# Performance work log

Hardware: AMD Instinct MI355X
Metric: run time of the kernel (lower is better)

The kernel has to match this reference:

```python
import jax, jax.numpy as jnp
import numpy as np

EPS = 1e-5

def setup_inputs() -> dict:
    key = jax.random.key(0)
    ks = jax.random.split(key, 5)
    B, C_clip, Hc, Wc = 8, 768, 24, 24
    C_rs, Hr, Wr = 256, 64, 64
    clip_feat = jax.random.normal(ks[0], (B, C_clip, Hc, Wc), dtype=jnp.float32)
    rs_feat = jax.random.normal(ks[1], (B, C_rs, Hr, Wr), dtype=jnp.float32)
    ln_gamma = jnp.ones((C_clip,), dtype=jnp.float32)
    ln_beta = jnp.zeros((C_clip,), dtype=jnp.float32)
    W = jax.random.normal(ks[2], (C_rs, C_clip), dtype=jnp.float32) * (1.0 / np.sqrt(C_clip))
    b = jax.random.normal(ks[3], (C_rs,), dtype=jnp.float32) * 0.01
    alpha = jnp.array([0.5], dtype=jnp.float32)
    return {"clip_feat": clip_feat, "rs_feat": rs_feat, "ln_gamma": ln_gamma,
            "ln_beta": ln_beta, "W": W, "b": b, "alpha": alpha}

def reference(clip_feat, rs_feat, ln_gamma, ln_beta, W, b, alpha):
    B, C_clip, Hc, Wc = clip_feat.shape
    _, C_rs, Hr, Wr = rs_feat.shape
    # tokens: [B, N_clip, C_clip]
    clip_flat = clip_feat.reshape(B, C_clip, Hc * Wc).transpose(0, 2, 1)
    mu = jnp.mean(clip_flat, axis=-1, keepdims=True)
    var = jnp.var(clip_flat, axis=-1, keepdims=True)
    clip_norm = (clip_flat - mu) * jax.lax.rsqrt(var + EPS) * ln_gamma + ln_beta
    # projection to rs_dim: [B, N_clip, C_rs]
    clip_proj = jnp.einsum('bnc,dc->bnd', clip_norm, W) + b
    # rs tokens: [B, N_rs, C_rs]
    rs_flat = rs_feat.reshape(B, C_rs, Hr * Wr).transpose(0, 2, 1)
    # attn_map: [B, N_clip, N_rs], softmax over N_clip (axis=1)
    attn = jnp.einsum('bnd,bmd->bnm', clip_proj, rs_flat)
    attn = jax.nn.softmax(attn, axis=1)
    # attended: [B, N_rs, C_rs]
    attended = jnp.einsum('bnm,bnd->bmd', attn, clip_proj)
    attended = attended.transpose(0, 2, 1).reshape(B, C_rs, Hr, Wr)
    return rs_feat + alpha * attended
```

## Files before the change

kernel.cpp:

```cpp
#include <hip/hip_runtime.h>
#include <hip/hip_bf16.h>

#define EPSF 1e-5f
#define SM_OFF 60.0f

typedef short short8 __attribute__((ext_vector_type(8)));
typedef float f32x4 __attribute__((ext_vector_type(4)));

__device__ __forceinline__ short f2bf(float x) {
    __hip_bfloat16 h = __float2bfloat16(x);
    return reinterpret_cast<short&>(h);
}
__device__ __forceinline__ float bf2f(short s) {
    __hip_bfloat16 h = reinterpret_cast<__hip_bfloat16&>(s);
    return __bfloat162float(h);
}
__device__ __forceinline__ unsigned int pk2(float lo, float hi) {
    return (unsigned int)(unsigned short)f2bf(lo)
         | ((unsigned int)(unsigned short)f2bf(hi) << 16);
}

__global__ __launch_bounds__(256) void w_pack_kernel(
    const float* __restrict__ W,
    short* __restrict__ Wp_hi,
    short* __restrict__ Wp_lo)
{
    int t = blockIdx.x * 256 + threadIdx.x;
    int l15 = t & 15;
    int g   = (t >> 4) & 3;
    int kt  = (t >> 6) % 24;
    int nt  = t / 1536;
    const float* src = W + (size_t)(16 * nt + l15) * 768 + 32 * kt + 8 * g;
    short8 h8, l8;
    #pragma unroll
    for (int j = 0; j < 8; ++j) {
        float w = src[j];
        short h = f2bf(w);
        h8[j] = h;
        l8[j] = f2bf(w - bf2f(h));
    }
    *reinterpret_cast<short8*>(Wp_hi + (size_t)t * 8) = h8;
    *reinterpret_cast<short8*>(Wp_lo + (size_t)t * 8) = l8;
}

__global__ __launch_bounds__(512) void ln_proj_kernel(
    const float* __restrict__ clip,
    const float* __restrict__ gamma,
    const float* __restrict__ beta,
    const short* __restrict__ Wp_hi,
    const short* __restrict__ Wp_lo,
    const float* __restrict__ bias,
    short* __restrict__ proj,
    short* __restrict__ projT)
{
    __shared__ short xh[16][776];
    __shared__ short xl[16][776];
    __shared__ float redA[8][16];
    __shared__ float redB[8][16];
    __shared__ float muS[16], rsS[16];

    const int tid = threadIdx.x;
    const int b  = blockIdx.x / 36;
    const int n0 = (blockIdx.x % 36) * 16;
    const int nl = tid & 15;
    const int cg = tid >> 4;
    const int w  = tid >> 6;
    const int l  = tid & 63;
    const int l15 = l & 15;
    const int g  = l >> 4;

    const float* base = clip + (size_t)b * 768 * 576 + n0 + nl;

    float x[24];
    float s1 = 0.f, s2 = 0.f;
    #pragma unroll
    for (int i = 0; i < 24; ++i) {
        x[i] = base[(size_t)(cg + 32 * i) * 576];
        s1 += x[i]; s2 += x[i] * x[i];
    }
    s1 += __shfl_xor(s1, 16); s2 += __shfl_xor(s2, 16);
    s1 += __shfl_xor(s1, 32); s2 += __shfl_xor(s2, 32);
    if (g == 0) { redA[w][l15] = s1; redB[w][l15] = s2; }
    __syncthreads();
    if (tid < 16) {
        float a = 0.f, q = 0.f;
        #pragma unroll
        for (int k = 0; k < 8; ++k) { a += redA[k][tid]; q += redB[k][tid]; }
        float mu = a * (1.f / 768.f);
        float var = q * (1.f / 768.f) - mu * mu;
        muS[tid] = mu; rsS[tid] = rsqrtf(var + EPSF);
    }
    __syncthreads();
    {
        float mu = muS[nl], rsg = rsS[nl];
        #pragma unroll
        for (int i = 0; i < 24; ++i) {
            int c = cg + 32 * i;
            float y = (x[i] - mu) * rsg * gamma[c] + beta[c];
            short hh = f2bf(y);
            xh[nl][c] = hh;
            xl[nl][c] = f2bf(y - bf2f(hh));
        }
    }
    __syncthreads();

    f32x4 acc[2];
    acc[0] = f32x4{0.f,0.f,0.f,0.f};
    acc[1] = f32x4{0.f,0.f,0.f,0.f};
    for (int kt = 0; kt < 24; ++kt) {
        short8 ah = *reinterpret_cast<const short8*>(&xh[l15][32 * kt + 8 * g]);
        short8 al = *reinterpret_cast<const short8*>(&xl[l15][32 * kt + 8 * g]);
        #pragma unroll
        for (int j = 0; j < 2; ++j) {
            int nt = 2 * w + j;
            size_t off = ((size_t)((nt * 24 + kt) * 64 + l)) * 8;
            short8 bh = *reinterpret_cast<const short8*>(Wp_hi + off);
            short8 bl = *reinterpret_cast<const short8*>(Wp_lo + off);
            acc[j] = __builtin_amdgcn_mfma_f32_16x16x32_bf16(ah, bh, acc[j], 0, 0, 0);
            acc[j] = __builtin_amdgcn_mfma_f32_16x16x32_bf16(al, bh, acc[j], 0, 0, 0);
            acc[j] = __builtin_amdgcn_mfma_f32_16x16x32_bf16(ah, bl, acc[j], 0, 0, 0);
        }
    }

    #pragma unroll
    for (int j = 0; j < 2; ++j) {
        int d = 16 * (2 * w + j) + l15;
        float bb = bias[d];
        #pragma unroll
        for (int r = 0; r < 4; ++r) {
            int tok = n0 + 4 * g + r;
            short v = f2bf(acc[j][r] + bb);
            proj[((size_t)b * 576 + tok) * 256 + d] = v;
            projT[((size_t)b * 256 + d) * 576 + tok] = v;
        }
    }
}

__global__ __launch_bounds__(256, 2) void attn_kernel(
    const short* __restrict__ proj,
    const short* __restrict__ projT,
    const float* __restrict__ rs,
    const float* __restrict__ alpha_p,
    float* __restrict__ out)
{
    __shared__ short Ks[2][32][264];
    __shared__ short VT[2][256][40];
    __shared__ unsigned int Ps[4][16][20];

    const int tid = threadIdx.x;
    const int b  = blockIdx.x >> 6;
    const int q0 = (blockIdx.x & 63) << 6;
    const int w   = tid >> 6;
    const int l   = tid & 63;
    const int l15 = l & 15;
    const int g   = l >> 4;
    const int qg  = q0 + 16 * w + l15;

    const short* kbase  = proj  + (size_t)b * 576 * 256;
    const short* ktbase = projT + (size_t)b * 256 * 576;
    const float* rbase  = rs + (size_t)b * 256 * 4096;
    float* obase = out + (size_t)b * 256 * 4096;

    short8 qf[8];
    #pragma unroll
    for (int dc = 0; dc < 8; ++dc) {
        short8 v;
        #pragma unroll
        for (int j = 0; j < 8; ++j)
            v[j] = f2bf(rbase[(size_t)(32 * dc + 8 * g + j) * 4096 + qg]);
        qf[dc] = v;
    }

    f32x4 acc[16];
    #pragma unroll
    for (int dt = 0; dt < 16; ++dt) acc[dt] = f32x4{0.f, 0.f, 0.f, 0.f};
    float rsum = 0.f;

    const int krow = tid >> 3, kc8 = tid & 7;
    short8 kpre[4], vpre[4];

    auto PREFETCH = [&](int c) {
        const short* ks = kbase + (size_t)(32 * c + krow) * 256 + kc8 * 32;
        #pragma unroll
        for (int j = 0; j < 4; ++j)
            kpre[j] = *reinterpret_cast<const short8*>(ks + 8 * j);
        const short* vs = ktbase + (size_t)tid * 576 + 32 * c;
        #pragma unroll
        for (int j = 0; j < 4; ++j)
            vpre[j] = *reinterpret_cast<const short8*>(vs + 8 * j);
    };
    auto WRITE = [&](int buf) {
        #pragma unroll
        for (int j = 0; j < 4; ++j)
            *reinterpret_cast<short8*>(&Ks[buf][krow][kc8 * 32 + 8 * j]) = kpre[j];
        #pragma unroll
        for (int j = 0; j < 4; ++j)
            *reinterpret_cast<short8*>(&VT[buf][tid][8 * j]) = vpre[j];
    };

    PREFETCH(0);
    WRITE(0);
    __syncthreads();

    for (int c = 0; c < 18; ++c) {
        const int cur = c & 1;
        if (c < 17) PREFETCH(c + 1);

        f32x4 s0{0.f,0.f,0.f,0.f}, s1{0.f,0.f,0.f,0.f};
        __builtin_amdgcn_s_setprio(1);
        #pragma unroll
        for (int dc = 0; dc < 8; ++dc) {
            short8 kf0 = *reinterpret_cast<const short8*>(&Ks[cur][l15][32 * dc + 8 * g]);
            short8 kf1 = *reinterpret_cast<const short8*>(&Ks[cur][16 + l15][32 * dc + 8 * g]);
            s0 = __builtin_amdgcn_mfma_f32_16x16x32_bf16(kf0, qf[dc], s0, 0, 0, 0);
            s1 = __builtin_amdgcn_mfma_f32_16x16x32_bf16(kf1, qf[dc], s1, 0, 0, 0);
        }
        __builtin_amdgcn_s_setprio(0);

        float p[8];
        #pragma unroll
        for (int r = 0; r < 4; ++r) {
            p[r]     = __expf(s0[r] - SM_OFF);
            p[4 + r] = __expf(s1[r] - SM_OFF);
        }
        #pragma unroll
        for (int r = 0; r < 8; ++r) rsum += p[r];

        unsigned int u0 = pk2(p[0], p[1]), u1 = pk2(p[2], p[3]);
        unsigned int u2 = pk2(p[4], p[5]), u3 = pk2(p[6], p[7]);
        *reinterpret_cast<uint2*>(&Ps[w][l15][2 * g])     = uint2{u0, u1};
        *reinterpret_cast<uint2*>(&Ps[w][l15][8 + 2 * g]) = uint2{u2, u3};

        short8 pf = *reinterpret_cast<const short8*>(&Ps[w][l15][4 * g]);
        __builtin_amdgcn_s_setprio(1);
        #pragma unroll
        for (int dt = 0; dt < 16; ++dt) {
            short8 vf = *reinterpret_cast<const short8*>(&VT[cur][16 * dt + l15][8 * g]);
            acc[dt] = __builtin_amdgcn_mfma_f32_16x16x32_bf16(vf, pf, acc[dt], 0, 0, 0);
        }
        __builtin_amdgcn_s_setprio(0);

        if (c < 17) {
            WRITE(cur ^ 1);
            __syncthreads();
        }
    }

    rsum += __shfl_xor(rsum, 16);
    rsum += __shfl_xor(rsum, 32);
    float inv = alpha_p[0] / rsum;

    #pragma unroll
    for (int dt = 0; dt < 16; ++dt) {
        #pragma unroll
        for (int r = 0; r < 4; ++r) {
            int d = 16 * dt + 4 * g + r;
            size_t idx = (size_t)d * 4096 + qg;
            obase[idx] = rbase[idx] + acc[dt][r] * inv;
        }
    }
}

extern "C" void kernel_launch(void* const* d_in, const int* in_sizes, int n_in,
                              void* d_out, int out_size, void* d_ws, size_t ws_size,
                              hipStream_t stream)
{
    const float* clip  = (const float*)d_in[0];
    const float* rsf   = (const float*)d_in[1];
    const float* gamma = (const float*)d_in[2];
    const float* beta  = (const float*)d_in[3];
    const float* W     = (const float*)d_in[4];
    const float* bias  = (const float*)d_in[5];
    const float* alpha = (const float*)d_in[6];
    float* out = (float*)d_out;

    char* ws = (char*)d_ws;
    short* Wp_hi = (short*)ws;
    short* Wp_lo = (short*)(ws + 393216);
    short* proj  = (short*)(ws + 786432);
    short* projT = (short*)(ws + 3145728);

    hipLaunchKernelGGL(w_pack_kernel, dim3(96), dim3(256), 0, stream, W, Wp_hi, Wp_lo);
    hipLaunchKernelGGL(ln_proj_kernel, dim3(288), dim3(512), 0, stream,
                       clip, gamma, beta, Wp_hi, Wp_lo, bias, proj, projT);
    hipLaunchKernelGGL(attn_kernel, dim3(512), dim3(256), 0, stream,
                       proj, projT, rsf, alpha, out);
}
```

Before: 77.00 us.

## Stage K tiles via direct global-to-LDS loads, read V from global, split projection blocks

The attention kernel now loads K chunks straight into a swizzled LDS buffer with global_load_lds instead of staging through registers. V fragments are read directly from global memory (projT) into registers each chunk rather than through an LDS copy. The projection kernel launches twice as many blocks, each computing half of the output columns, which doubles the LayerNorm work but gives more parallelism. Risks are global-load latency on V sitting on the critical path, redundant LN computation, and the correctness of the swizzle and LDS layout.

```diff
diff --git a/kernel.cpp b/kernel.cpp
--- a/kernel.cpp
+++ b/kernel.cpp
@@ -18,6 +18,12 @@
 __device__ __forceinline__ unsigned int pk2(float lo, float hi) {
     return (unsigned int)(unsigned short)f2bf(lo)
          | ((unsigned int)(unsigned short)f2bf(hi) << 16);
+}
+__device__ __forceinline__ void gload_lds16(const short* g, short* lds) {
+    __builtin_amdgcn_global_load_lds(
+        (const __attribute__((address_space(1))) unsigned int*)g,
+        (__attribute__((address_space(3))) unsigned int*)lds,
+        16, 0, 0);
 }
 
 __global__ __launch_bounds__(256) void w_pack_kernel(
@@ -60,8 +66,10 @@
     __shared__ float muS[16], rsS[16];
 
     const int tid = threadIdx.x;
-    const int b  = blockIdx.x / 36;
-    const int n0 = (blockIdx.x % 36) * 16;
+    const int bb = blockIdx.x >> 1;
+    const int dh = blockIdx.x & 1;
+    const int b  = bb / 36;
+    const int n0 = (bb % 36) * 16;
     const int nl = tid & 15;
     const int cg = tid >> 4;
     const int w  = tid >> 6;
@@ -104,32 +112,26 @@
     }
     __syncthreads();
 
-    f32x4 acc[2];
-    acc[0] = f32x4{0.f,0.f,0.f,0.f};
-    acc[1] = f32x4{0.f,0.f,0.f,0.f};
+    const int nt = 8 * dh + w;
+    f32x4 acc = f32x4{0.f, 0.f, 0.f, 0.f};
     for (int kt = 0; kt < 24; ++kt) {
         short8 ah = *reinterpret_cast<const short8*>(&xh[l15][32 * kt + 8 * g]);
         short8 al = *reinterpret_cast<const short8*>(&xl[l15][32 * kt + 8 * g]);
-        #pragma unroll
-        for (int j = 0; j < 2; ++j) {
-            int nt = 2 * w + j;
-            size_t off = ((size_t)((nt * 24 + kt) * 64 + l)) * 8;
-            short8 bh = *reinterpret_cast<const short8*>(Wp_hi + off);
-            short8 bl = *reinterpret_cast<const short8*>(Wp_lo + off);
-            acc[j] = __builtin_amdgcn_mfma_f32_16x16x32_bf16(ah, bh, acc[j], 0, 0, 0);
-            acc[j] = __builtin_amdgcn_mfma_f32_16x16x32_bf16(al, bh, acc[j], 0, 0, 0);
-            acc[j] = __builtin_amdgcn_mfma_f32_16x16x32_bf16(ah, bl, acc[j], 0, 0, 0);
-        }
-    }
-
-    #pragma unroll
-    for (int j = 0; j < 2; ++j) {
-        int d = 16 * (2 * w + j) + l15;
-        float bb = bias[d];
+        size_t off = ((size_t)((nt * 24 + kt) * 64 + l)) * 8;
+        short8 bh = *reinterpret_cast<const short8*>(Wp_hi + off);
+        short8 bl = *reinterpret_cast<const short8*>(Wp_lo + off);
+        acc = __builtin_amdgcn_mfma_f32_16x16x32_bf16(ah, bh, acc, 0, 0, 0);
+        acc = __builtin_amdgcn_mfma_f32_16x16x32_bf16(al, bh, acc, 0, 0, 0);
+        acc = __builtin_amdgcn_mfma_f32_16x16x32_bf16(ah, bl, acc, 0, 0, 0);
+    }
+
+    {
+        int d = 16 * nt + l15;
+        float bb2 = bias[d];
         #pragma unroll
         for (int r = 0; r < 4; ++r) {
             int tok = n0 + 4 * g + r;
-            short v = f2bf(acc[j][r] + bb);
+            short v = f2bf(acc[r] + bb2);
             proj[((size_t)b * 576 + tok) * 256 + d] = v;
             projT[((size_t)b * 256 + d) * 576 + tok] = v;
         }
@@ -143,8 +145,7 @@
     const float* __restrict__ alpha_p,
     float* __restrict__ out)
 {
-    __shared__ short Ks[2][32][264];
-    __shared__ short VT[2][256][40];
+    __shared__ short Ks[2][32][256];
     __shared__ unsigned int Ps[4][16][20];
 
     const int tid = threadIdx.x;
@@ -176,42 +177,36 @@
     for (int dt = 0; dt < 16; ++dt) acc[dt] = f32x4{0.f, 0.f, 0.f, 0.f};
     float rsum = 0.f;
 
-    const int krow = tid >> 3, kc8 = tid & 7;
-    short8 kpre[4], vpre[4];
-
-    auto PREFETCH = [&](int c) {
-        const short* ks = kbase + (size_t)(32 * c + krow) * 256 + kc8 * 32;
-        #pragma unroll
-        for (int j = 0; j < 4; ++j)
-            kpre[j] = *reinterpret_cast<const short8*>(ks + 8 * j);
-        const short* vs = ktbase + (size_t)tid * 576 + 32 * c;
-        #pragma unroll
-        for (int j = 0; j < 4; ++j)
-            vpre[j] = *reinterpret_cast<const short8*>(vs + 8 * j);
+    auto STAGE = [&](int c, int buf) {
+        #pragma unroll
+        for (int i = 0; i < 4; ++i) {
+            int rr = 8 * w + 2 * i + (l >> 5);
+            const short* src = kbase + ((size_t)(32 * c + rr) << 8)
+                             + ((((l & 31) ^ (rr & 7))) << 3);
+            gload_lds16(src, &Ks[buf][8 * w + 2 * i][0]);
+        }
     };
-    auto WRITE = [&](int buf) {
-        #pragma unroll
-        for (int j = 0; j < 4; ++j)
-            *reinterpret_cast<short8*>(&Ks[buf][krow][kc8 * 32 + 8 * j]) = kpre[j];
-        #pragma unroll
-        for (int j = 0; j < 4; ++j)
-            *reinterpret_cast<short8*>(&VT[buf][tid][8 * j]) = vpre[j];
-    };
-
-    PREFETCH(0);
-    WRITE(0);
+
+    STAGE(0, 0);
     __syncthreads();
 
     for (int c = 0; c < 18; ++c) {
         const int cur = c & 1;
-        if (c < 17) PREFETCH(c + 1);
+        if (c < 17) STAGE(c + 1, cur ^ 1);
+
+        short8 vf[16];
+        #pragma unroll
+        for (int dt = 0; dt < 16; ++dt)
+            vf[dt] = *reinterpret_cast<const short8*>(
+                ktbase + (size_t)(16 * dt + l15) * 576 + 32 * c + 8 * g);
 
         f32x4 s0{0.f,0.f,0.f,0.f}, s1{0.f,0.f,0.f,0.f};
         __builtin_amdgcn_s_setprio(1);
         #pragma unroll
         for (int dc = 0; dc < 8; ++dc) {
-            short8 kf0 = *reinterpret_cast<const short8*>(&Ks[cur][l15][32 * dc + 8 * g]);
-            short8 kf1 = *reinterpret_cast<const short8*>(&Ks[cur][16 + l15][32 * dc + 8 * g]);
+            int sw = (((4 * dc + g) ^ (l15 & 7))) * 8;
+            short8 kf0 = *reinterpret_cast<const short8*>(&Ks[cur][l15][sw]);
+            short8 kf1 = *reinterpret_cast<const short8*>(&Ks[cur][16 + l15][sw]);
             s0 = __builtin_amdgcn_mfma_f32_16x16x32_bf16(kf0, qf[dc], s0, 0, 0, 0);
             s1 = __builtin_amdgcn_mfma_f32_16x16x32_bf16(kf1, qf[dc], s1, 0, 0, 0);
         }
@@ -234,16 +229,11 @@
         short8 pf = *reinterpret_cast<const short8*>(&Ps[w][l15][4 * g]);
         __builtin_amdgcn_s_setprio(1);
         #pragma unroll
-        for (int dt = 0; dt < 16; ++dt) {
-            short8 vf = *reinterpret_cast<const short8*>(&VT[cur][16 * dt + l15][8 * g]);
-            acc[dt] = __builtin_amdgcn_mfma_f32_16x16x32_bf16(vf, pf, acc[dt], 0, 0, 0);
-        }
+        for (int dt = 0; dt < 16; ++dt)
+            acc[dt] = __builtin_amdgcn_mfma_f32_16x16x32_bf16(vf[dt], pf, acc[dt], 0, 0, 0);
         __builtin_amdgcn_s_setprio(0);
 
-        if (c < 17) {
-            WRITE(cur ^ 1);
-            __syncthreads();
-        }
+        if (c < 17) __syncthreads();
     }
 
     rsum += __shfl_xor(rsum, 16);
@@ -281,7 +271,7 @@
     short* projT = (short*)(ws + 3145728);
 
     hipLaunchKernelGGL(w_pack_kernel, dim3(96), dim3(256), 0, stream, W, Wp_hi, Wp_lo);
-    hipLaunchKernelGGL(ln_proj_kernel, dim3(288), dim3(512), 0, stream,
+    hipLaunchKernelGGL(ln_proj_kernel, dim3(576), dim3(512), 0, stream,
                        clip, gamma, beta, Wp_hi, Wp_lo, bias, proj, projT);
     hipLaunchKernelGGL(attn_kernel, dim3(512), dim3(256), 0, stream,
                        proj, projT, rsf, alpha, out);
```

Result: slower. 110.8 us (+43.8%).
